# Kernel tuning notes

Hardware: AMD Instinct MI355X
Metric: run time of the kernel (lower is better)

The kernel has to match this reference:

```python
import jax, jax.numpy as jnp
import numpy as np

PI2 = 6.283185307


def setup_inputs() -> dict:
    key = jax.random.key(0)
    k1, k2, k3, k4 = jax.random.split(key, 4)
    T, n_mix, n_dim = 262144, 64, 16
    data = jax.random.normal(k1, (T, n_dim), dtype=jnp.float32)
    # mixture weights: positive, roughly summing to 1
    wghts = jax.random.uniform(k2, (n_mix, 1), dtype=jnp.float32, minval=0.5, maxval=1.5) / n_mix
    means = jax.random.normal(k3, (n_mix, n_dim), dtype=jnp.float32)
    # diagonal covariances: strictly positive
    dcovs = jax.random.uniform(k4, (n_mix, n_dim), dtype=jnp.float32, minval=0.5, maxval=1.5)
    return {"data": data, "wghts": wghts, "means": means, "dcovs": dcovs}


def reference(data, wghts, means, dcovs):
    # data: (T, D); wghts: (M, 1); means: (M, D); dcovs: (M, D)
    n_dim = data.shape[1]
    c = 1.0 / np.sqrt(PI2 ** n_dim)  # Gaussian normalizer (2*pi)^{-D/2}
    c_dets = 1.0 / jnp.sqrt(jnp.prod(dcovs, axis=1))  # (M,) |Sigma|^{-1/2}
    dprecs = 1.0 / dcovs  # (M, D) diagonal precisions
    diff = data[:, None, :] - means[None, :, :]  # (T, M, D)
    mhbs_dist = jnp.einsum('tmd,md->tm', diff * diff, dprecs)  # (T, M)
    probs = (wghts[:, 0] * c * c_dets)[None, :] * jnp.exp(-0.5 * mhbs_dist)  # (T, M)
    likes = jnp.sum(probs, axis=1)  # (T,)
    log_likes = jnp.mean(jnp.log(likes))
    posteriors = probs / likes[:, None]  # (T, M)
    e_means = posteriors @ means  # (T, D) weighted mean of component means
    return (log_likes, e_means)
```

## Files before the change

kernel.cpp:

```cpp
#include <hip/hip_runtime.h>

#define T_TOTAL 262144
#define NBLOCKS 2048
#define NMIX 64
#define NDIM 16

typedef short bf16x8 __attribute__((ext_vector_type(8)));
typedef unsigned short u16x8 __attribute__((ext_vector_type(8)));
typedef unsigned short u16x4 __attribute__((ext_vector_type(4)));
typedef float f32x4 __attribute__((ext_vector_type(4)));

__device__ __forceinline__ unsigned short f2bf(float f) {
    union { float f; unsigned u; } v; v.f = f;
    unsigned r = v.u + 0x7fff + ((v.u >> 16) & 1);
    return (unsigned short)(r >> 16);
}
__device__ __forceinline__ float bf2f(unsigned short s) {
    union { unsigned u; float f; } v; v.u = ((unsigned)s) << 16;
    return v.f;
}

#define L_WH   0
#define L_WL   5120
#define L_MUT  10240
#define L_A2   12544
#define L_RED  12800
#define L_F    12864
#define L_P    31296

__global__ __launch_bounds__(256, 4) void gmm_main(const float* __restrict__ data,
                                                   const float* __restrict__ wghts,
                                                   const float* __restrict__ means,
                                                   const float* __restrict__ dcovs,
                                                   float* __restrict__ out,
                                                   float* __restrict__ part) {
    __shared__ __align__(16) char lds[40512];
    const int tid  = threadIdx.x;
    const int w    = tid >> 6;
    const int lane = tid & 63;
    const int gi   = lane & 15;
    const int gq   = lane >> 4;
    const size_t tblk = (size_t)blockIdx.x * 128;

    const int row = tid >> 1, half = tid & 1;
    const float4* xp = (const float4*)(data + (tblk + row) * 16 + half * 8);
    float4 xa = xp[0], xb = xp[1];

    {
        const int m  = tid >> 2;
        const int ql = tid & 3;
        const float LOG2E = 1.4426950408889634f;
        const float LOG2_2PI = 2.6514961294723187f;
        const float4 d4 = *(const float4*)(dcovs + m * 16 + ql * 4);
        const float4 m4 = *(const float4*)(means + m * 16 + ql * 4);
        const float wm = wghts[m];
        float dc[4] = {d4.x, d4.y, d4.z, d4.w};
        float mu[4] = {m4.x, m4.y, m4.z, m4.w};
        u16x4 ghv, glv, hhv, hlv;
        float sumlog = 0.0f, qsum = 0.0f;
        unsigned short* mut = (unsigned short*)(lds + L_MUT);
#pragma unroll
        for (int j = 0; j < 4; ++j) {
            float pr = __builtin_amdgcn_rcpf(dc[j]);
            float g = -0.5f * LOG2E * pr;
            float h = LOG2E * pr * mu[j];
            unsigned short gH = f2bf(g), hH = f2bf(h);
            ghv[j] = gH;  glv[j] = f2bf(g - bf2f(gH));
            hhv[j] = hH;  hlv[j] = f2bf(h - bf2f(hH));
            mut[(ql * 4 + j) * 72 + m] = f2bf(mu[j]);
            sumlog += __builtin_amdgcn_logf(dc[j]);
            qsum   += pr * mu[j] * mu[j];
        }
        char* wrh = lds + L_WH + m * 80;
        char* wrl = lds + L_WL + m * 80;
        *(u16x4*)(wrh + ql * 8)      = ghv;
        *(u16x4*)(wrh + 32 + ql * 8) = hhv;
        *(u16x4*)(wrl + ql * 8)      = glv;
        *(u16x4*)(wrl + 32 + ql * 8) = hlv;
        sumlog += __shfl_xor(sumlog, 1); sumlog += __shfl_xor(sumlog, 2);
        qsum   += __shfl_xor(qsum, 1);   qsum   += __shfl_xor(qsum, 2);
        if (ql == 0) {
            float log2C = __builtin_amdgcn_logf(wm) - 8.0f * LOG2_2PI - 0.5f * sumlog;
            ((float*)(lds + L_A2))[m] = log2C - 0.5f * LOG2E * qsum;
        }
    }

    {
        int fw = row >> 5, lr = row & 31;
        float xv[8] = {xa.x, xa.y, xa.z, xa.w, xb.x, xb.y, xb.z, xb.w};
        u16x8 vh2, vl2, vhx, vlx;
#pragma unroll
        for (int d = 0; d < 8; ++d) {
            float q = xv[d] * xv[d];
            unsigned short qh = f2bf(q);
            vh2[d] = qh;               vl2[d] = f2bf(q - bf2f(qh));
            unsigned short xh = f2bf(xv[d]);
            vhx[d] = xh;               vlx[d] = f2bf(xv[d] - bf2f(xh));
        }
        char* fb = lds + L_F + fw * 4608 + lr * 144;
        *(u16x8*)(fb + half * 16)        = vh2;
        *(u16x8*)(fb + 32 + half * 16)   = vhx;
        *(u16x8*)(fb + 64 + half * 16)   = vl2;
        *(u16x8*)(fb + 96 + half * 16)   = vlx;
    }
    __syncthreads();

    bf16x8 bh[4], bl[4];
    float a2v[4];
#pragma unroll
    for (int c = 0; c < 4; ++c) {
        bh[c] = *(const bf16x8*)(lds + L_WH + (c * 16 + gi) * 80 + gq * 16);
        bl[c] = *(const bf16x8*)(lds + L_WL + (c * 16 + gi) * 80 + gq * 16);
        a2v[c] = ((const float*)(lds + L_A2))[c * 16 + gi];
    }
    bf16x8 mf0 = *(const bf16x8*)(lds + L_MUT + gi * 144 + gq * 16);
    bf16x8 mf1 = *(const bf16x8*)(lds + L_MUT + gi * 144 + 64 + gq * 16);

    const char* fbase = lds + L_F + w * 4608;
    char* pbase = lds + L_P + w * 2304;
    float ll_acc = 0.0f;

#pragma unroll
    for (int rt = 0; rt < 2; ++rt) {
        bf16x8 ah = *(const bf16x8*)(fbase + (rt * 16 + gi) * 144 + gq * 16);
        bf16x8 al = *(const bf16x8*)(fbase + (rt * 16 + gi) * 144 + 64 + gq * 16);

        f32x4 pacc[4];
#pragma unroll
        for (int c = 0; c < 4; ++c) {
            f32x4 a = {0.0f, 0.0f, 0.0f, 0.0f};
            a = __builtin_amdgcn_mfma_f32_16x16x32_bf16(al, bh[c], a, 0, 0, 0);
            a = __builtin_amdgcn_mfma_f32_16x16x32_bf16(ah, bl[c], a, 0, 0, 0);
            a = __builtin_amdgcn_mfma_f32_16x16x32_bf16(ah, bh[c], a, 0, 0, 0);
            pacc[c] = a;
        }

        float p[4][4], prow[4], inv[4];
#pragma unroll
        for (int reg = 0; reg < 4; ++reg) {
#pragma unroll
            for (int c = 0; c < 4; ++c)
                p[c][reg] = __builtin_amdgcn_exp2f(pacc[c][reg] + a2v[c]);
            prow[reg] = (p[0][reg] + p[1][reg]) + (p[2][reg] + p[3][reg]);
        }
#pragma unroll
        for (int reg = 0; reg < 4; ++reg) {
            float v = prow[reg];
            v += __shfl_xor(v, 1);  v += __shfl_xor(v, 2);
            v += __shfl_xor(v, 4);  v += __shfl_xor(v, 8);
            v = fmaxf(v, 1e-35f);
            ll_acc += __builtin_amdgcn_logf(v);
            inv[reg] = __builtin_amdgcn_rcpf(v);
        }

#pragma unroll
        for (int c = 0; c < 4; ++c)
#pragma unroll
            for (int reg = 0; reg < 4; ++reg)
                *(unsigned short*)(pbase + (gq * 4 + reg) * 144 + (c * 16 + gi) * 2) =
                    f2bf(p[c][reg]);

        bf16x8 ap0 = *(const bf16x8*)(pbase + gi * 144 + gq * 16);
        bf16x8 ap1 = *(const bf16x8*)(pbase + gi * 144 + 64 + gq * 16);
        f32x4 e = {0.0f, 0.0f, 0.0f, 0.0f};
        e = __builtin_amdgcn_mfma_f32_16x16x32_bf16(ap0, mf0, e, 0, 0, 0);
        e = __builtin_amdgcn_mfma_f32_16x16x32_bf16(ap1, mf1, e, 0, 0, 0);

        size_t trow = tblk + (size_t)w * 32 + rt * 16 + gq * 4;
#pragma unroll
        for (int reg = 0; reg < 4; ++reg)
            out[1 + (trow + reg) * 16 + gi] = e[reg] * inv[reg];
    }

    ll_acc += __shfl_xor(ll_acc, 16);
    ll_acc += __shfl_xor(ll_acc, 32);
    if (lane == 0) ((float*)(lds + L_RED))[w] = ll_acc;
    __syncthreads();
    if (tid == 0) {
        float* r = (float*)(lds + L_RED);
        part[blockIdx.x] = (r[0] + r[1]) + (r[2] + r[3]);
    }
}

__global__ void gmm_fin(const float* __restrict__ part, float* __restrict__ out) {
    __shared__ double red[4];
    const int tid = threadIdx.x;
    double s = 0.0;
#pragma unroll
    for (int k = 0; k < 8; ++k) s += (double)part[tid + k * 256];
#pragma unroll
    for (int off = 32; off > 0; off >>= 1) s += __shfl_down(s, off, 64);
    const int wv = tid >> 6, lane = tid & 63;
    if (lane == 0) red[wv] = s;
    __syncthreads();
    if (tid == 0) {
        const double LN2 = 0.6931471805599453;
        double tot = (red[0] + red[1]) + (red[2] + red[3]);
        out[0] = (float)(tot * LN2 / (double)T_TOTAL);
    }
}

extern "C" void kernel_launch(void* const* d_in, const int* in_sizes, int n_in,
                              void* d_out, int out_size, void* d_ws, size_t ws_size,
                              hipStream_t stream) {
    const float* data  = (const float*)d_in[0];
    const float* wghts = (const float*)d_in[1];
    const float* means = (const float*)d_in[2];
    const float* dcovs = (const float*)d_in[3];
    float* out  = (float*)d_out;
    float* part = (float*)d_ws;

    gmm_main<<<NBLOCKS, 256, 0, stream>>>(data, wghts, means, dcovs, out, part);
    gmm_fin<<<1, 256, 0, stream>>>(part, out);
}
```

Baseline: 86.40 us.

## Load data rows directly into MFMA fragments and double the rows per block

Each lane now reads its slice of the data row straight from global memory in MFMA A-fragment layout and converts it to split bf16 in registers. This drops the LDS staging buffer for features, and the next tile's load is issued before the current tile is computed. Blocks now cover 256 rows with 4 tiles per wave and half as many blocks, so the per-block parameter setup is amortised over more rows. The risks are fewer blocks to hide latency and lane-strided global loads that are less coalesced.

```diff
diff --git a/kernel.cpp b/kernel.cpp
--- a/kernel.cpp
+++ b/kernel.cpp
@@ -1,7 +1,7 @@
 #include <hip/hip_runtime.h>
 
 #define T_TOTAL 262144
-#define NBLOCKS 2048
+#define NBLOCKS 1024
 #define NMIX 64
 #define NDIM 16
 
@@ -25,8 +25,7 @@
 #define L_MUT  10240
 #define L_A2   12544
 #define L_RED  12800
-#define L_F    12864
-#define L_P    31296
+#define L_P    12864
 
 __global__ __launch_bounds__(256, 4) void gmm_main(const float* __restrict__ data,
                                                    const float* __restrict__ wghts,
@@ -34,17 +33,13 @@
                                                    const float* __restrict__ dcovs,
                                                    float* __restrict__ out,
                                                    float* __restrict__ part) {
-    __shared__ __align__(16) char lds[40512];
+    __shared__ __align__(16) char lds[22080];
     const int tid  = threadIdx.x;
     const int w    = tid >> 6;
     const int lane = tid & 63;
     const int gi   = lane & 15;
     const int gq   = lane >> 4;
-    const size_t tblk = (size_t)blockIdx.x * 128;
-
-    const int row = tid >> 1, half = tid & 1;
-    const float4* xp = (const float4*)(data + (tblk + row) * 16 + half * 8);
-    float4 xa = xp[0], xb = xp[1];
+    const size_t tblk = (size_t)blockIdx.x * 256;
 
     {
         const int m  = tid >> 2;
@@ -84,25 +79,6 @@
             ((float*)(lds + L_A2))[m] = log2C - 0.5f * LOG2E * qsum;
         }
     }
-
-    {
-        int fw = row >> 5, lr = row & 31;
-        float xv[8] = {xa.x, xa.y, xa.z, xa.w, xb.x, xb.y, xb.z, xb.w};
-        u16x8 vh2, vl2, vhx, vlx;
-#pragma unroll
-        for (int d = 0; d < 8; ++d) {
-            float q = xv[d] * xv[d];
-            unsigned short qh = f2bf(q);
-            vh2[d] = qh;               vl2[d] = f2bf(q - bf2f(qh));
-            unsigned short xh = f2bf(xv[d]);
-            vhx[d] = xh;               vlx[d] = f2bf(xv[d] - bf2f(xh));
-        }
-        char* fb = lds + L_F + fw * 4608 + lr * 144;
-        *(u16x8*)(fb + half * 16)        = vh2;
-        *(u16x8*)(fb + 32 + half * 16)   = vhx;
-        *(u16x8*)(fb + 64 + half * 16)   = vl2;
-        *(u16x8*)(fb + 96 + half * 16)   = vlx;
-    }
     __syncthreads();
 
     bf16x8 bh[4], bl[4];
@@ -116,14 +92,33 @@
     bf16x8 mf0 = *(const bf16x8*)(lds + L_MUT + gi * 144 + gq * 16);
     bf16x8 mf1 = *(const bf16x8*)(lds + L_MUT + gi * 144 + 64 + gq * 16);
 
-    const char* fbase = lds + L_F + w * 4608;
     char* pbase = lds + L_P + w * 2304;
     float ll_acc = 0.0f;
 
-#pragma unroll
-    for (int rt = 0; rt < 2; ++rt) {
-        bf16x8 ah = *(const bf16x8*)(fbase + (rt * 16 + gi) * 144 + gq * 16);
-        bf16x8 al = *(const bf16x8*)(fbase + (rt * 16 + gi) * 144 + 64 + gq * 16);
+    const float* xbase = data + (tblk + (size_t)w * 64 + gi) * 16 + (gq & 1) * 8;
+    float4 xa = *(const float4*)(xbase);
+    float4 xb = *(const float4*)(xbase + 4);
+    const bool sq = (gq < 2);
+
+#pragma unroll
+    for (int rt = 0; rt < 4; ++rt) {
+        float4 na, nb;
+        if (rt < 3) {
+            na = *(const float4*)(xbase + (rt + 1) * 256);
+            nb = *(const float4*)(xbase + (rt + 1) * 256 + 4);
+        }
+
+        float xv[8] = {xa.x, xa.y, xa.z, xa.w, xb.x, xb.y, xb.z, xb.w};
+        u16x8 ahv, alv;
+#pragma unroll
+        for (int j = 0; j < 8; ++j) {
+            float q = sq ? xv[j] * xv[j] : xv[j];
+            unsigned short qh = f2bf(q);
+            ahv[j] = qh;
+            alv[j] = f2bf(q - bf2f(qh));
+        }
+        bf16x8 ah = *(bf16x8*)&ahv;
+        bf16x8 al = *(bf16x8*)&alv;
 
         f32x4 pacc[4];
 #pragma unroll
@@ -166,10 +161,12 @@
         e = __builtin_amdgcn_mfma_f32_16x16x32_bf16(ap0, mf0, e, 0, 0, 0);
         e = __builtin_amdgcn_mfma_f32_16x16x32_bf16(ap1, mf1, e, 0, 0, 0);
 
-        size_t trow = tblk + (size_t)w * 32 + rt * 16 + gq * 4;
+        size_t trow = tblk + (size_t)w * 64 + rt * 16 + gq * 4;
 #pragma unroll
         for (int reg = 0; reg < 4; ++reg)
             out[1 + (trow + reg) * 16 + gi] = e[reg] * inv[reg];
+
+        if (rt < 3) { xa = na; xb = nb; }
     }
 
     ll_acc += __shfl_xor(ll_acc, 16);
@@ -187,7 +184,7 @@
     const int tid = threadIdx.x;
     double s = 0.0;
 #pragma unroll
-    for (int k = 0; k < 8; ++k) s += (double)part[tid + k * 256];
+    for (int k = 0; k < 4; ++k) s += (double)part[tid + k * 256];
 #pragma unroll
     for (int off = 32; off > 0; off >>= 1) s += __shfl_down(s, off, 64);
     const int wv = tid >> 6, lane = tid & 63;
```

Measured after the change: 82.79 us. 1.04x faster.
